# Performance work log

Hardware: AMD Instinct MI355X
Metric: run time of the kernel (lower is better)

The kernel has to match this reference:

```python
import jax, jax.numpy as jnp
import numpy as np

B, T, D, H = 4096, 512, 8, 64  # batch, seq_len, input_size, hidden_size


def setup_inputs() -> dict:
    key = jax.random.key(0)
    ks = jax.random.split(key, 11)
    s = lambda k, shape: (jax.random.normal(k, shape, dtype=jnp.float32) * 0.1)
    return {
        "x": jax.random.normal(ks[0], (B, T, D), dtype=jnp.float32),
        # layer 0 (input_size -> H), PyTorch gate order i,f,g,o packed along 4H
        "Wih0": s(ks[1], (4 * H, D)),
        "Whh0": s(ks[2], (4 * H, H)),
        "bih0": s(ks[3], (4 * H,)),
        "bhh0": s(ks[4], (4 * H,)),
        # layer 1 (H -> H)
        "Wih1": s(ks[5], (4 * H, H)),
        "Whh1": s(ks[6], (4 * H, H)),
        "bih1": s(ks[7], (4 * H,)),
        "bhh1": s(ks[8], (4 * H,)),
        # final linear head H -> 1
        "Wfc": s(ks[9], (1, H)),
        "bfc": s(ks[10], (1,)),
    }


def _lstm_layer(x, Wih, Whh, bih, bhh):
    """Single-direction LSTM layer over x:[B,T,Din] -> hs:[B,T,H]."""
    b, t, _ = x.shape
    h_dim = Whh.shape[1]
    # Precompute input contribution for all timesteps (one big GEMM).
    xg = jnp.einsum("btd,gd->btg", x, Wih) + bih + bhh  # [B,T,4H]

    def step(carry, gx_t):
        h, c = carry
        z = gx_t + h @ Whh.T  # [B,4H]
        i, f, g, o = jnp.split(z, 4, axis=-1)
        i = jax.nn.sigmoid(i)
        f = jax.nn.sigmoid(f)
        g = jnp.tanh(g)
        o = jax.nn.sigmoid(o)
        c = f * c + i * g
        h = o * jnp.tanh(c)
        return (h, c), h

    h0 = jnp.zeros((b, h_dim), x.dtype)
    c0 = jnp.zeros((b, h_dim), x.dtype)
    (_, _), hs = jax.lax.scan(step, (h0, c0), jnp.swapaxes(xg, 0, 1))
    return jnp.swapaxes(hs, 0, 1)  # [B,T,H]


def reference(x, Wih0, Whh0, bih0, bhh0, Wih1, Whh1, bih1, bhh1, Wfc, bfc):
    # nn.LSTM with num_layers=2, batch_first=True; dropout inactive in eval.
    h1 = _lstm_layer(x, Wih0, Whh0, bih0, bhh0)
    h2 = _lstm_layer(h1, Wih1, Whh1, bih1, bhh1)
    last = h2[:, -1, :]  # [B,H]
    return last @ Wfc.T + bfc  # [B,1]
```

## Files before the change

### kernel.cpp

```cpp
#include <hip/hip_runtime.h>

#define BTOT 4096
#define TB   512
#define BD   8
#define BSL  16

#define A0TOG  1024
#define A1BASE 2048
#define A1TOG  1024
#define ZBASE  4096
#define XBASE  8192
#define NLDS   24576

typedef __attribute__((ext_vector_type(8))) short  short8;
typedef __attribute__((ext_vector_type(4))) float  f32x4;

static __device__ __forceinline__ unsigned short f2bf(float f) {
    unsigned u = __float_as_uint(f);
    u += 0x7fffu + ((u >> 16) & 1u);
    return (unsigned short)(u >> 16);
}
static __device__ __forceinline__ float bf2f(unsigned short h) {
    return __uint_as_float(((unsigned)h) << 16);
}
static __device__ __forceinline__ unsigned pkbf(float a, float b) {
    unsigned r;
    asm("v_cvt_pk_bf16_f32 %0, %1, %2" : "=v"(r) : "v"(a), "v"(b));
    return r;
}

static __device__ __forceinline__ void gates4(
    const f32x4 ai, const f32x4 af, const f32x4 ag, const f32x4 ao,
    float cc[4], unsigned hp[2])
{
    float h[4];
    #pragma unroll
    for (int r = 0; r < 4; ++r) {
        const float ei = __builtin_amdgcn_exp2f(ai[r]);
        const float ef = __builtin_amdgcn_exp2f(af[r]);
        const float eg = __builtin_amdgcn_exp2f(ag[r]);
        const float eo = __builtin_amdgcn_exp2f(ao[r]);
        const float Ai = 1.f + ei, Af = 1.f + ef, Ag = 1.f + eg, Ao = 1.f + eo;
        const float P    = Ai * Ag;
        const float numer = cc[r] * P + Af * (eg - 1.f);
        const float rD   = __builtin_amdgcn_rcpf(Af * P);
        cc[r] = numer * rD;
        const float ec = __builtin_amdgcn_exp2f(2.88539008f * cc[r]);
        const float rH = __builtin_amdgcn_rcpf(Ao * (ec + 1.f));
        h[r] = (ec - 1.f) * rH;
    }
    hp[0] = pkbf(h[0], h[1]); hp[1] = pkbf(h[2], h[3]);
}

__global__ __launch_bounds__(512, 2) void lstm2_fused(
    const float* __restrict__ x,
    const float* __restrict__ Wih0, const float* __restrict__ Whh0,
    const float* __restrict__ bih0, const float* __restrict__ bhh0,
    const float* __restrict__ Wih1, const float* __restrict__ Whh1,
    const float* __restrict__ bih1, const float* __restrict__ bhh1,
    const float* __restrict__ Wfc,  const float* __restrict__ bfc,
    float* __restrict__ out)
{
    __shared__ __align__(16) unsigned short lds16[NLDS];

    const int tid  = threadIdx.x;
    const int wid  = tid >> 6;
    const int lane = tid & 63;
    const int q    = lane >> 4;
    const int ln   = lane & 15;
    const int rb   = blockIdx.x * BSL;

    const bool L1w = (wid >= 4);
    const int  g   = L1w ? (wid - 4) : wid;
    const int  jc  = g * 16 + ln;

    const float SCI = -1.44269504f;
    const float SCG =  2.88539008f;
    short8 Bf[4][4];
    #pragma unroll
    for (int G = 0; G < 4; ++G) {
        const int n = G * 64 + jc;
        const float sc = (G == 2) ? SCG : SCI;
        #pragma unroll
        for (int ki = 0; ki < 4; ++ki) {
            union { unsigned short u[8]; short8 v; } t;
            #pragma unroll
            for (int j = 0; j < 8; ++j) {
                const int k = ki * 32 + q * 8 + j;
                float wv = 0.0f;
                if (!L1w) {
                    if (ki < 3) {
                        if (k < 64)      wv = Whh0[n * 64 + k];
                        else if (k < 72) wv = Wih0[n * 8 + (k - 64)];
                    }
                } else {
                    if (k < 64)          wv = Wih1[n * 64 + k];
                    else                 wv = Whh1[n * 64 + (k - 64)];
                }
                t.u[j] = f2bf(sc * wv);
            }
            Bf[G][ki] = t.v;
        }
    }
    f32x4 biasv[4];
    #pragma unroll
    for (int G = 0; G < 4; ++G) {
        const int n = G * 64 + jc;
        const float sc = (G == 2) ? SCG : SCI;
        const float b = sc * (L1w ? (bih1[n] + bhh1[n]) : (bih0[n] + bhh0[n]));
        biasv[G] = (f32x4){b, b, b, b};
    }

    {
        unsigned* z = (unsigned*)lds16;
        #pragma unroll
        for (int i = 0; i < 5; ++i) {
            const int id = tid + i * 512;
            if (id < 2112) z[id] = 0;
        }
    }
    const int srow = tid >> 5, su = tid & 31;
    {
        const float* gp = x + (size_t)(rb + srow) * (TB * BD) + su * 16;
        const float4 v0 = ((const float4*)gp)[0];
        const float4 v1 = ((const float4*)gp)[1];
        const float4 v2 = ((const float4*)gp)[2];
        const float4 v3 = ((const float4*)gp)[3];
        uint4 s0, s1;
        s0.x = pkbf(v0.x, v0.y); s0.y = pkbf(v0.z, v0.w);
        s0.z = pkbf(v1.x, v1.y); s0.w = pkbf(v1.z, v1.w);
        s1.x = pkbf(v2.x, v2.y); s1.y = pkbf(v2.z, v2.w);
        s1.z = pkbf(v3.x, v3.y); s1.w = pkbf(v3.z, v3.w);
        const int el = XBASE + (su * 2) * 128 + srow * 8;
        *(uint4*)(lds16 + el)       = s0;
        *(uint4*)(lds16 + el + 128) = s1;
    }
    __syncthreads();

    const int rbase = q * 128 + ln * 8;
    const int wb    = (jc >> 3) * 128 + q * 32 + (jc & 7);
    const int ln8   = ln * 8;
    const int zaddr = ZBASE + ln8;
    int rdA  = rbase;
    int wr0  = A0TOG + wb;
    int rdH0 = rbase;
    int rdH1 = A1BASE + rbase;
    int wrH1 = A1BASE + A1TOG + wb;

    float cc[4] = {0.f, 0.f, 0.f, 0.f};
    float4 px0, px1, px2, px3;

    for (int it = 0; it <= TB; ++it) {
        const int ph = it & 63;
        if (ph == 48 && it + 16 < TB) {
            const int t0 = (it & ~63) + 64;
            const float* gp = x + (size_t)(rb + srow) * (TB * BD) + t0 * BD + su * 16;
            px0 = ((const float4*)gp)[0];
            px1 = ((const float4*)gp)[1];
            px2 = ((const float4*)gp)[2];
            px3 = ((const float4*)gp)[3];
        }
        if (ph == 62 && it + 2 < TB) {
            const int t0 = (it & ~63) + 64;
            uint4 s0, s1;
            s0.x = pkbf(px0.x, px0.y); s0.y = pkbf(px0.z, px0.w);
            s0.z = pkbf(px1.x, px1.y); s0.w = pkbf(px1.z, px1.w);
            s1.x = pkbf(px2.x, px2.y); s1.y = pkbf(px2.z, px2.w);
            s1.z = pkbf(px3.x, px3.y); s1.w = pkbf(px3.z, px3.w);
            const int el = XBASE + ((t0 & 127) + su * 2) * 128 + srow * 8;
            *(uint4*)(lds16 + el)       = s0;
            *(uint4*)(lds16 + el + 128) = s1;
        }

        if (!L1w) {
            if (it < TB) {
                const short8 a0 = *(const short8*)(lds16 + rdA);
                const short8 a1 = *(const short8*)(lds16 + rdA + 512);
                const int xaddr = (q == 0) ? (XBASE + ((it & 127) << 7) + ln8) : zaddr;
                const short8 a2 = *(const short8*)(lds16 + xaddr);

                f32x4 ai = __builtin_amdgcn_mfma_f32_16x16x32_bf16(a0, Bf[0][0], biasv[0], 0, 0, 0);
                f32x4 af = __builtin_amdgcn_mfma_f32_16x16x32_bf16(a0, Bf[1][0], biasv[1], 0, 0, 0);
                f32x4 ag = __builtin_amdgcn_mfma_f32_16x16x32_bf16(a0, Bf[2][0], biasv[2], 0, 0, 0);
                f32x4 ao = __builtin_amdgcn_mfma_f32_16x16x32_bf16(a0, Bf[3][0], biasv[3], 0, 0, 0);
                ai = __builtin_amdgcn_mfma_f32_16x16x32_bf16(a1, Bf[0][1], ai, 0, 0, 0);
                af = __builtin_amdgcn_mfma_f32_16x16x32_bf16(a1, Bf[1][1], af, 0, 0, 0);
                ag = __builtin_amdgcn_mfma_f32_16x16x32_bf16(a1, Bf[2][1], ag, 0, 0, 0);
                ao = __builtin_amdgcn_mfma_f32_16x16x32_bf16(a1, Bf[3][1], ao, 0, 0, 0);
                ai = __builtin_amdgcn_mfma_f32_16x16x32_bf16(a2, Bf[0][2], ai, 0, 0, 0);
                af = __builtin_amdgcn_mfma_f32_16x16x32_bf16(a2, Bf[1][2], af, 0, 0, 0);
                ag = __builtin_amdgcn_mfma_f32_16x16x32_bf16(a2, Bf[2][2], ag, 0, 0, 0);
                ao = __builtin_amdgcn_mfma_f32_16x16x32_bf16(a2, Bf[3][2], ao, 0, 0, 0);

                unsigned hp[2];
                gates4(ai, af, ag, ao, cc, hp);
                lds16[wr0]      = (unsigned short)hp[0];
                lds16[wr0 + 8]  = (unsigned short)(hp[0] >> 16);
                lds16[wr0 + 16] = (unsigned short)hp[1];
                lds16[wr0 + 24] = (unsigned short)(hp[1] >> 16);
            }
        } else {
            if (it >= 1) {
                const short8 a0 = *(const short8*)(lds16 + rdH0);
                const short8 a1 = *(const short8*)(lds16 + rdH0 + 512);
                const short8 a2 = *(const short8*)(lds16 + rdH1);
                const short8 a3 = *(const short8*)(lds16 + rdH1 + 512);

                f32x4 ai = __builtin_amdgcn_mfma_f32_16x16x32_bf16(a0, Bf[0][0], biasv[0], 0, 0, 0);
                f32x4 af = __builtin_amdgcn_mfma_f32_16x16x32_bf16(a0, Bf[1][0], biasv[1], 0, 0, 0);
                f32x4 ag = __builtin_amdgcn_mfma_f32_16x16x32_bf16(a0, Bf[2][0], biasv[2], 0, 0, 0);
                f32x4 ao = __builtin_amdgcn_mfma_f32_16x16x32_bf16(a0, Bf[3][0], biasv[3], 0, 0, 0);
                ai = __builtin_amdgcn_mfma_f32_16x16x32_bf16(a1, Bf[0][1], ai, 0, 0, 0);
                af = __builtin_amdgcn_mfma_f32_16x16x32_bf16(a1, Bf[1][1], af, 0, 0, 0);
                ag = __builtin_amdgcn_mfma_f32_16x16x32_bf16(a1, Bf[2][1], ag, 0, 0, 0);
                ao = __builtin_amdgcn_mfma_f32_16x16x32_bf16(a1, Bf[3][1], ao, 0, 0, 0);
                ai = __builtin_amdgcn_mfma_f32_16x16x32_bf16(a2, Bf[0][2], ai, 0, 0, 0);
                af = __builtin_amdgcn_mfma_f32_16x16x32_bf16(a2, Bf[1][2], af, 0, 0, 0);
                ag = __builtin_amdgcn_mfma_f32_16x16x32_bf16(a2, Bf[2][2], ag, 0, 0, 0);
                ao = __builtin_amdgcn_mfma_f32_16x16x32_bf16(a2, Bf[3][2], ao, 0, 0, 0);
                ai = __builtin_amdgcn_mfma_f32_16x16x32_bf16(a3, Bf[0][3], ai, 0, 0, 0);
                af = __builtin_amdgcn_mfma_f32_16x16x32_bf16(a3, Bf[1][3], af, 0, 0, 0);
                ag = __builtin_amdgcn_mfma_f32_16x16x32_bf16(a3, Bf[2][3], ag, 0, 0, 0);
                ao = __builtin_amdgcn_mfma_f32_16x16x32_bf16(a3, Bf[3][3], ao, 0, 0, 0);

                unsigned hp[2];
                gates4(ai, af, ag, ao, cc, hp);
                lds16[wrH1]      = (unsigned short)hp[0];
                lds16[wrH1 + 8]  = (unsigned short)(hp[0] >> 16);
                lds16[wrH1 + 16] = (unsigned short)hp[1];
                lds16[wrH1 + 24] = (unsigned short)(hp[1] >> 16);
            }
        }
        __syncthreads();
        rdA ^= A0TOG; wr0 ^= A0TOG; rdH0 ^= A0TOG;
        rdH1 ^= A1TOG; wrH1 ^= A1TOG;
    }

    if (tid < BSL) {
        float s = bfc[0];
        #pragma unroll 8
        for (int j = 0; j < 64; ++j)
            s += bf2f(lds16[A1BASE + A1TOG + (j >> 3) * 128 + tid * 8 + (j & 7)]) * Wfc[j];
        out[rb + tid] = s;
    }
}

extern "C" void kernel_launch(void* const* d_in, const int* in_sizes, int n_in,
                              void* d_out, int out_size, void* d_ws, size_t ws_size,
                              hipStream_t stream) {
    const float* x    = (const float*)d_in[0];
    const float* Wih0 = (const float*)d_in[1];
    const float* Whh0 = (const float*)d_in[2];
    const float* bih0 = (const float*)d_in[3];
    const float* bhh0 = (const float*)d_in[4];
    const float* Wih1 = (const float*)d_in[5];
    const float* Whh1 = (const float*)d_in[6];
    const float* bih1 = (const float*)d_in[7];
    const float* bhh1 = (const float*)d_in[8];
    const float* Wfc  = (const float*)d_in[9];
    const float* bfc  = (const float*)d_in[10];
    float* out = (float*)d_out;

    dim3 grid(BTOT / BSL);
    dim3 block(512);
    lstm2_fused<<<grid, block, 0, stream>>>(x, Wih0, Whh0, bih0, bhh0,
                                            Wih1, Whh1, bih1, bhh1, Wfc, bfc, out);
}
```

Measured before the change: 504.6 us.

## Merge both LSTM layers into each wave with 256-thread blocks and peeled loop

Each wave now computes both layer-0 and layer-1 gates for its hidden-column slice instead of splitting layers across wave groups, which halves the block to 256 threads. The first and last timesteps are peeled out of the loop to remove per-iteration branching. __syncthreads is replaced with an explicit lgkmcnt wait plus s_barrier. The change cuts barrier participants and lets the two layers' MFMA chains interleave within one wave, but it doubles the weight registers per thread and uses launch bounds of one block, so occupancy and register pressure may suffer.

```diff
diff --git a/kernel.cpp b/kernel.cpp
--- a/kernel.cpp
+++ b/kernel.cpp
@@ -14,6 +14,10 @@
 
 typedef __attribute__((ext_vector_type(8))) short  short8;
 typedef __attribute__((ext_vector_type(4))) float  f32x4;
+
+#define MFMA16 __builtin_amdgcn_mfma_f32_16x16x32_bf16
+
+#define BAR() asm volatile("s_waitcnt lgkmcnt(0)\n\ts_barrier" ::: "memory")
 
 static __device__ __forceinline__ unsigned short f2bf(float f) {
     unsigned u = __float_as_uint(f);
@@ -52,7 +56,7 @@
     hp[0] = pkbf(h[0], h[1]); hp[1] = pkbf(h[2], h[3]);
 }
 
-__global__ __launch_bounds__(512, 2) void lstm2_fused(
+__global__ __launch_bounds__(256, 1) void lstm2_fused(
     const float* __restrict__ x,
     const float* __restrict__ Wih0, const float* __restrict__ Whh0,
     const float* __restrict__ bih0, const float* __restrict__ bhh0,
@@ -69,71 +73,76 @@
     const int q    = lane >> 4;
     const int ln   = lane & 15;
     const int rb   = blockIdx.x * BSL;
-
-    const bool L1w = (wid >= 4);
-    const int  g   = L1w ? (wid - 4) : wid;
-    const int  jc  = g * 16 + ln;
+    const int jc   = wid * 16 + ln;
 
     const float SCI = -1.44269504f;
     const float SCG =  2.88539008f;
-    short8 Bf[4][4];
+
+    short8 Bf0[4][3];
+    short8 Bf1[4][4];
     #pragma unroll
     for (int G = 0; G < 4; ++G) {
         const int n = G * 64 + jc;
         const float sc = (G == 2) ? SCG : SCI;
+        #pragma unroll
+        for (int ki = 0; ki < 3; ++ki) {
+            union { unsigned short u[8]; short8 v; } t;
+            #pragma unroll
+            for (int j = 0; j < 8; ++j) {
+                const int k = ki * 32 + q * 8 + j;
+                float wv = 0.0f;
+                if (k < 64)      wv = Whh0[n * 64 + k];
+                else if (k < 72) wv = Wih0[n * 8 + (k - 64)];
+                t.u[j] = f2bf(sc * wv);
+            }
+            Bf0[G][ki] = t.v;
+        }
         #pragma unroll
         for (int ki = 0; ki < 4; ++ki) {
             union { unsigned short u[8]; short8 v; } t;
             #pragma unroll
             for (int j = 0; j < 8; ++j) {
                 const int k = ki * 32 + q * 8 + j;
-                float wv = 0.0f;
-                if (!L1w) {
-                    if (ki < 3) {
-                        if (k < 64)      wv = Whh0[n * 64 + k];
-                        else if (k < 72) wv = Wih0[n * 8 + (k - 64)];
-                    }
-                } else {
-                    if (k < 64)          wv = Wih1[n * 64 + k];
-                    else                 wv = Whh1[n * 64 + (k - 64)];
-                }
+                const float wv = (k < 64) ? Wih1[n * 64 + k]
+                                          : Whh1[n * 64 + (k - 64)];
                 t.u[j] = f2bf(sc * wv);
             }
-            Bf[G][ki] = t.v;
-        }
-    }
-    f32x4 biasv[4];
+            Bf1[G][ki] = t.v;
+        }
+    }
+    f32x4 bias0[4], bias1[4];
     #pragma unroll
     for (int G = 0; G < 4; ++G) {
         const int n = G * 64 + jc;
         const float sc = (G == 2) ? SCG : SCI;
-        const float b = sc * (L1w ? (bih1[n] + bhh1[n]) : (bih0[n] + bhh0[n]));
-        biasv[G] = (f32x4){b, b, b, b};
+        const float b0 = sc * (bih0[n] + bhh0[n]);
+        const float b1 = sc * (bih1[n] + bhh1[n]);
+        bias0[G] = (f32x4){b0, b0, b0, b0};
+        bias1[G] = (f32x4){b1, b1, b1, b1};
     }
 
     {
         unsigned* z = (unsigned*)lds16;
         #pragma unroll
-        for (int i = 0; i < 5; ++i) {
-            const int id = tid + i * 512;
+        for (int i = 0; i < 9; ++i) {
+            const int id = tid + i * 256;
             if (id < 2112) z[id] = 0;
         }
     }
-    const int srow = tid >> 5, su = tid & 31;
+    const int srow = tid >> 4, su = tid & 15;
     {
-        const float* gp = x + (size_t)(rb + srow) * (TB * BD) + su * 16;
-        const float4 v0 = ((const float4*)gp)[0];
-        const float4 v1 = ((const float4*)gp)[1];
-        const float4 v2 = ((const float4*)gp)[2];
-        const float4 v3 = ((const float4*)gp)[3];
-        uint4 s0, s1;
-        s0.x = pkbf(v0.x, v0.y); s0.y = pkbf(v0.z, v0.w);
-        s0.z = pkbf(v1.x, v1.y); s0.w = pkbf(v1.z, v1.w);
-        s1.x = pkbf(v2.x, v2.y); s1.y = pkbf(v2.z, v2.w);
-        s1.z = pkbf(v3.x, v3.y); s1.w = pkbf(v3.z, v3.w);
-        const int el = XBASE + (su * 2) * 128 + srow * 8;
-        *(uint4*)(lds16 + el)       = s0;
-        *(uint4*)(lds16 + el + 128) = s1;
+        const float* gp = x + (size_t)(rb + srow) * (TB * BD) + su * 32;
+        float4 v[8];
+        #pragma unroll
+        for (int i = 0; i < 8; ++i) v[i] = ((const float4*)gp)[i];
+        #pragma unroll
+        for (int tt = 0; tt < 4; ++tt) {
+            uint4 s;
+            s.x = pkbf(v[2*tt].x,   v[2*tt].y);   s.y = pkbf(v[2*tt].z,   v[2*tt].w);
+            s.z = pkbf(v[2*tt+1].x, v[2*tt+1].y); s.w = pkbf(v[2*tt+1].z, v[2*tt+1].w);
+            const int el = XBASE + (su * 4 + tt) * 128 + srow * 8;
+            *(uint4*)(lds16 + el) = s;
+        }
     }
     __syncthreads();
 
@@ -143,97 +152,142 @@
     const int zaddr = ZBASE + ln8;
     int rdA  = rbase;
     int wr0  = A0TOG + wb;
-    int rdH0 = rbase;
     int rdH1 = A1BASE + rbase;
     int wrH1 = A1BASE + A1TOG + wb;
 
-    float cc[4] = {0.f, 0.f, 0.f, 0.f};
-    float4 px0, px1, px2, px3;
-
-    for (int it = 0; it <= TB; ++it) {
+    float cc0[4] = {0.f, 0.f, 0.f, 0.f};
+    float cc1[4] = {0.f, 0.f, 0.f, 0.f};
+    float4 px[8];
+
+    {
+        const short8 a0 = *(const short8*)(lds16 + rdA);
+        const short8 a1 = *(const short8*)(lds16 + rdA + 512);
+        const int xaddr = (q == 0) ? (XBASE + 0 + ln8) : zaddr;
+        const short8 a2 = *(const short8*)(lds16 + xaddr);
+        f32x4 ai = MFMA16(a0, Bf0[0][0], bias0[0], 0, 0, 0);
+        f32x4 af = MFMA16(a0, Bf0[1][0], bias0[1], 0, 0, 0);
+        f32x4 ag = MFMA16(a0, Bf0[2][0], bias0[2], 0, 0, 0);
+        f32x4 ao = MFMA16(a0, Bf0[3][0], bias0[3], 0, 0, 0);
+        ai = MFMA16(a1, Bf0[0][1], ai, 0, 0, 0);
+        af = MFMA16(a1, Bf0[1][1], af, 0, 0, 0);
+        ag = MFMA16(a1, Bf0[2][1], ag, 0, 0, 0);
+        ao = MFMA16(a1, Bf0[3][1], ao, 0, 0, 0);
+        ai = MFMA16(a2, Bf0[0][2], ai, 0, 0, 0);
+        af = MFMA16(a2, Bf0[1][2], af, 0, 0, 0);
+        ag = MFMA16(a2, Bf0[2][2], ag, 0, 0, 0);
+        ao = MFMA16(a2, Bf0[3][2], ao, 0, 0, 0);
+        unsigned hp[2];
+        gates4(ai, af, ag, ao, cc0, hp);
+        lds16[wr0]      = (unsigned short)hp[0];
+        lds16[wr0 + 8]  = (unsigned short)(hp[0] >> 16);
+        lds16[wr0 + 16] = (unsigned short)hp[1];
+        lds16[wr0 + 24] = (unsigned short)(hp[1] >> 16);
+        BAR();
+        rdA ^= A0TOG; wr0 ^= A0TOG; rdH1 ^= A1TOG; wrH1 ^= A1TOG;
+    }
+
+    for (int it = 1; it < TB; ++it) {
         const int ph = it & 63;
         if (ph == 48 && it + 16 < TB) {
             const int t0 = (it & ~63) + 64;
-            const float* gp = x + (size_t)(rb + srow) * (TB * BD) + t0 * BD + su * 16;
-            px0 = ((const float4*)gp)[0];
-            px1 = ((const float4*)gp)[1];
-            px2 = ((const float4*)gp)[2];
-            px3 = ((const float4*)gp)[3];
+            const float* gp = x + (size_t)(rb + srow) * (TB * BD) + t0 * BD + su * 32;
+            #pragma unroll
+            for (int i = 0; i < 8; ++i) px[i] = ((const float4*)gp)[i];
         }
         if (ph == 62 && it + 2 < TB) {
             const int t0 = (it & ~63) + 64;
-            uint4 s0, s1;
-            s0.x = pkbf(px0.x, px0.y); s0.y = pkbf(px0.z, px0.w);
-            s0.z = pkbf(px1.x, px1.y); s0.w = pkbf(px1.z, px1.w);
-            s1.x = pkbf(px2.x, px2.y); s1.y = pkbf(px2.z, px2.w);
-            s1.z = pkbf(px3.x, px3.y); s1.w = pkbf(px3.z, px3.w);
-            const int el = XBASE + ((t0 & 127) + su * 2) * 128 + srow * 8;
-            *(uint4*)(lds16 + el)       = s0;
-            *(uint4*)(lds16 + el + 128) = s1;
-        }
-
-        if (!L1w) {
-            if (it < TB) {
-                const short8 a0 = *(const short8*)(lds16 + rdA);
-                const short8 a1 = *(const short8*)(lds16 + rdA + 512);
-                const int xaddr = (q == 0) ? (XBASE + ((it & 127) << 7) + ln8) : zaddr;
-                const short8 a2 = *(const short8*)(lds16 + xaddr);
-
-                f32x4 ai = __builtin_amdgcn_mfma_f32_16x16x32_bf16(a0, Bf[0][0], biasv[0], 0, 0, 0);
-                f32x4 af = __builtin_amdgcn_mfma_f32_16x16x32_bf16(a0, Bf[1][0], biasv[1], 0, 0, 0);
-                f32x4 ag = __builtin_amdgcn_mfma_f32_16x16x32_bf16(a0, Bf[2][0], biasv[2], 0, 0, 0);
-                f32x4 ao = __builtin_amdgcn_mfma_f32_16x16x32_bf16(a0, Bf[3][0], biasv[3], 0, 0, 0);
-                ai = __builtin_amdgcn_mfma_f32_16x16x32_bf16(a1, Bf[0][1], ai, 0, 0, 0);
-                af = __builtin_amdgcn_mfma_f32_16x16x32_bf16(a1, Bf[1][1], af, 0, 0, 0);
-                ag = __builtin_amdgcn_mfma_f32_16x16x32_bf16(a1, Bf[2][1], ag, 0, 0, 0);
-                ao = __builtin_amdgcn_mfma_f32_16x16x32_bf16(a1, Bf[3][1], ao, 0, 0, 0);
-                ai = __builtin_amdgcn_mfma_f32_16x16x32_bf16(a2, Bf[0][2], ai, 0, 0, 0);
-                af = __builtin_amdgcn_mfma_f32_16x16x32_bf16(a2, Bf[1][2], af, 0, 0, 0);
-                ag = __builtin_amdgcn_mfma_f32_16x16x32_bf16(a2, Bf[2][2], ag, 0, 0, 0);
-                ao = __builtin_amdgcn_mfma_f32_16x16x32_bf16(a2, Bf[3][2], ao, 0, 0, 0);
-
-                unsigned hp[2];
-                gates4(ai, af, ag, ao, cc, hp);
-                lds16[wr0]      = (unsigned short)hp[0];
-                lds16[wr0 + 8]  = (unsigned short)(hp[0] >> 16);
-                lds16[wr0 + 16] = (unsigned short)hp[1];
-                lds16[wr0 + 24] = (unsigned short)(hp[1] >> 16);
+            #pragma unroll
+            for (int tt = 0; tt < 4; ++tt) {
+                uint4 s;
+                s.x = pkbf(px[2*tt].x,   px[2*tt].y);   s.y = pkbf(px[2*tt].z,   px[2*tt].w);
+                s.z = pkbf(px[2*tt+1].x, px[2*tt+1].y); s.w = pkbf(px[2*tt+1].z, px[2*tt+1].w);
+                const int el = XBASE + ((t0 + su * 4 + tt) & 127) * 128 + srow * 8;
+                *(uint4*)(lds16 + el) = s;
             }
-        } else {
-            if (it >= 1) {
-                const short8 a0 = *(const short8*)(lds16 + rdH0);
-                const short8 a1 = *(const short8*)(lds16 + rdH0 + 512);
-                const short8 a2 = *(const short8*)(lds16 + rdH1);
-                const short8 a3 = *(const short8*)(lds16 + rdH1 + 512);
-
-                f32x4 ai = __builtin_amdgcn_mfma_f32_16x16x32_bf16(a0, Bf[0][0], biasv[0], 0, 0, 0);
-                f32x4 af = __builtin_amdgcn_mfma_f32_16x16x32_bf16(a0, Bf[1][0], biasv[1], 0, 0, 0);
-                f32x4 ag = __builtin_amdgcn_mfma_f32_16x16x32_bf16(a0, Bf[2][0], biasv[2], 0, 0, 0);
-                f32x4 ao = __builtin_amdgcn_mfma_f32_16x16x32_bf16(a0, Bf[3][0], biasv[3], 0, 0, 0);
-                ai = __builtin_amdgcn_mfma_f32_16x16x32_bf16(a1, Bf[0][1], ai, 0, 0, 0);
-                af = __builtin_amdgcn_mfma_f32_16x16x32_bf16(a1, Bf[1][1], af, 0, 0, 0);
-                ag = __builtin_amdgcn_mfma_f32_16x16x32_bf16(a1, Bf[2][1], ag, 0, 0, 0);
-                ao = __builtin_amdgcn_mfma_f32_16x16x32_bf16(a1, Bf[3][1], ao, 0, 0, 0);
-                ai = __builtin_amdgcn_mfma_f32_16x16x32_bf16(a2, Bf[0][2], ai, 0, 0, 0);
-                af = __builtin_amdgcn_mfma_f32_16x16x32_bf16(a2, Bf[1][2], af, 0, 0, 0);
-                ag = __builtin_amdgcn_mfma_f32_16x16x32_bf16(a2, Bf[2][2], ag, 0, 0, 0);
-                ao = __builtin_amdgcn_mfma_f32_16x16x32_bf16(a2, Bf[3][2], ao, 0, 0, 0);
-                ai = __builtin_amdgcn_mfma_f32_16x16x32_bf16(a3, Bf[0][3], ai, 0, 0, 0);
-                af = __builtin_amdgcn_mfma_f32_16x16x32_bf16(a3, Bf[1][3], af, 0, 0, 0);
-                ag = __builtin_amdgcn_mfma_f32_16x16x32_bf16(a3, Bf[2][3], ag, 0, 0, 0);
-                ao = __builtin_amdgcn_mfma_f32_16x16x32_bf16(a3, Bf[3][3], ao, 0, 0, 0);
-
-                unsigned hp[2];
-                gates4(ai, af, ag, ao, cc, hp);
-                lds16[wrH1]      = (unsigned short)hp[0];
-                lds16[wrH1 + 8]  = (unsigned short)(hp[0] >> 16);
-                lds16[wrH1 + 16] = (unsigned short)hp[1];
-                lds16[wrH1 + 24] = (unsigned short)(hp[1] >> 16);
-            }
-        }
-        __syncthreads();
-        rdA ^= A0TOG; wr0 ^= A0TOG; rdH0 ^= A0TOG;
-        rdH1 ^= A1TOG; wrH1 ^= A1TOG;
+        }
+
+        const short8 a0 = *(const short8*)(lds16 + rdA);
+        const short8 a1 = *(const short8*)(lds16 + rdA + 512);
+        const short8 b2 = *(const short8*)(lds16 + rdH1);
+        const short8 b3 = *(const short8*)(lds16 + rdH1 + 512);
+        const int xaddr = (q == 0) ? (XBASE + ((it & 127) << 7) + ln8) : zaddr;
+        const short8 a2 = *(const short8*)(lds16 + xaddr);
+
+        f32x4 ai0 = MFMA16(a0, Bf0[0][0], bias0[0], 0, 0, 0);
+        f32x4 af0 = MFMA16(a0, Bf0[1][0], bias0[1], 0, 0, 0);
+        f32x4 ag0 = MFMA16(a0, Bf0[2][0], bias0[2], 0, 0, 0);
+        f32x4 ao0 = MFMA16(a0, Bf0[3][0], bias0[3], 0, 0, 0);
+        ai0 = MFMA16(a1, Bf0[0][1], ai0, 0, 0, 0);
+        af0 = MFMA16(a1, Bf0[1][1], af0, 0, 0, 0);
+        ag0 = MFMA16(a1, Bf0[2][1], ag0, 0, 0, 0);
+        ao0 = MFMA16(a1, Bf0[3][1], ao0, 0, 0, 0);
+        ai0 = MFMA16(a2, Bf0[0][2], ai0, 0, 0, 0);
+        af0 = MFMA16(a2, Bf0[1][2], af0, 0, 0, 0);
+        ag0 = MFMA16(a2, Bf0[2][2], ag0, 0, 0, 0);
+        ao0 = MFMA16(a2, Bf0[3][2], ao0, 0, 0, 0);
+
+        f32x4 ai1 = MFMA16(a0, Bf1[0][0], bias1[0], 0, 0, 0);
+        f32x4 af1 = MFMA16(a0, Bf1[1][0], bias1[1], 0, 0, 0);
+        f32x4 ag1 = MFMA16(a0, Bf1[2][0], bias1[2], 0, 0, 0);
+        f32x4 ao1 = MFMA16(a0, Bf1[3][0], bias1[3], 0, 0, 0);
+        ai1 = MFMA16(a1, Bf1[0][1], ai1, 0, 0, 0);
+        af1 = MFMA16(a1, Bf1[1][1], af1, 0, 0, 0);
+        ag1 = MFMA16(a1, Bf1[2][1], ag1, 0, 0, 0);
+        ao1 = MFMA16(a1, Bf1[3][1], ao1, 0, 0, 0);
+        ai1 = MFMA16(b2, Bf1[0][2], ai1, 0, 0, 0);
+        af1 = MFMA16(b2, Bf1[1][2], af1, 0, 0, 0);
+        ag1 = MFMA16(b2, Bf1[2][2], ag1, 0, 0, 0);
+        ao1 = MFMA16(b2, Bf1[3][2], ao1, 0, 0, 0);
+        ai1 = MFMA16(b3, Bf1[0][3], ai1, 0, 0, 0);
+        af1 = MFMA16(b3, Bf1[1][3], af1, 0, 0, 0);
+        ag1 = MFMA16(b3, Bf1[2][3], ag1, 0, 0, 0);
+        ao1 = MFMA16(b3, Bf1[3][3], ao1, 0, 0, 0);
+
+        unsigned hp0[2], hp1[2];
+        gates4(ai0, af0, ag0, ao0, cc0, hp0);
+        lds16[wr0]      = (unsigned short)hp0[0];
+        lds16[wr0 + 8]  = (unsigned short)(hp0[0] >> 16);
+        lds16[wr0 + 16] = (unsigned short)hp0[1];
+        lds16[wr0 + 24] = (unsigned short)(hp0[1] >> 16);
+
+        gates4(ai1, af1, ag1, ao1, cc1, hp1);
+        lds16[wrH1]      = (unsigned short)hp1[0];
+        lds16[wrH1 + 8]  = (unsigned short)(hp1[0] >> 16);
+        lds16[wrH1 + 16] = (unsigned short)hp1[1];
+        lds16[wrH1 + 24] = (unsigned short)(hp1[1] >> 16);
+
+        BAR();
+        rdA ^= A0TOG; wr0 ^= A0TOG; rdH1 ^= A1TOG; wrH1 ^= A1TOG;
+    }
+
+    {
+        const short8 a0 = *(const short8*)(lds16 + rdA);
+        const short8 a1 = *(const short8*)(lds16 + rdA + 512);
+        const short8 b2 = *(const short8*)(lds16 + rdH1);
+        const short8 b3 = *(const short8*)(lds16 + rdH1 + 512);
+        f32x4 ai = MFMA16(a0, Bf1[0][0], bias1[0], 0, 0, 0);
+        f32x4 af = MFMA16(a0, Bf1[1][0], bias1[1], 0, 0, 0);
+        f32x4 ag = MFMA16(a0, Bf1[2][0], bias1[2], 0, 0, 0);
+        f32x4 ao = MFMA16(a0, Bf1[3][0], bias1[3], 0, 0, 0);
+        ai = MFMA16(a1, Bf1[0][1], ai, 0, 0, 0);
+        af = MFMA16(a1, Bf1[1][1], af, 0, 0, 0);
+        ag = MFMA16(a1, Bf1[2][1], ag, 0, 0, 0);
+        ao = MFMA16(a1, Bf1[3][1], ao, 0, 0, 0);
+        ai = MFMA16(b2, Bf1[0][2], ai, 0, 0, 0);
+        af = MFMA16(b2, Bf1[1][2], af, 0, 0, 0);
+        ag = MFMA16(b2, Bf1[2][2], ag, 0, 0, 0);
+        ao = MFMA16(b2, Bf1[3][2], ao, 0, 0, 0);
+        ai = MFMA16(b3, Bf1[0][3], ai, 0, 0, 0);
+        af = MFMA16(b3, Bf1[1][3], af, 0, 0, 0);
+        ag = MFMA16(b3, Bf1[2][3], ag, 0, 0, 0);
+        ao = MFMA16(b3, Bf1[3][3], ao, 0, 0, 0);
+        unsigned hp[2];
+        gates4(ai, af, ag, ao, cc1, hp);
+        lds16[wrH1]      = (unsigned short)hp[0];
+        lds16[wrH1 + 8]  = (unsigned short)(hp[0] >> 16);
+        lds16[wrH1 + 16] = (unsigned short)hp[1];
+        lds16[wrH1 + 24] = (unsigned short)(hp[1] >> 16);
+        BAR();
     }
 
     if (tid < BSL) {
@@ -262,7 +316,7 @@
     float* out = (float*)d_out;
 
     dim3 grid(BTOT / BSL);
-    dim3 block(512);
+    dim3 block(256);
     lstm2_fused<<<grid, block, 0, stream>>>(x, Wih0, Whh0, bih0, bhh0,
                                             Wih1, Whh1, bih1, bhh1, Wfc, bfc, out);
 }
```

New measurement: 503.6 us. No clear change (-0.2%).

## Split LSTM step into MFMA and gate phases, interleaving layer-0 and layer-1 waves

Applied to the files above, without the earlier changes.

Each time step now has two barrier-separated phases. Layer-0 waves run their MFMAs in the first phase and gate math in the second, while layer-1 waves do the reverse, so matrix and transcendental work from the two layers overlap across waves. The layer-1 pipeline is skewed by one more step, and __syncthreads is replaced with an explicit lgkmcnt wait plus s_barrier. In exchange there are two barriers per step instead of one, the loop runs one extra iteration, and the accumulator registers stay live across the barrier.

```diff
diff --git a/kernel.cpp b/kernel.cpp
--- a/kernel.cpp
+++ b/kernel.cpp
@@ -14,6 +14,10 @@
 
 typedef __attribute__((ext_vector_type(8))) short  short8;
 typedef __attribute__((ext_vector_type(4))) float  f32x4;
+
+#define MFMA16 __builtin_amdgcn_mfma_f32_16x16x32_bf16
+
+#define BAR() asm volatile("s_waitcnt lgkmcnt(0)\n\ts_barrier" ::: "memory")
 
 static __device__ __forceinline__ unsigned short f2bf(float f) {
     unsigned u = __float_as_uint(f);
@@ -76,6 +80,7 @@
 
     const float SCI = -1.44269504f;
     const float SCG =  2.88539008f;
+
     short8 Bf[4][4];
     #pragma unroll
     for (int G = 0; G < 4; ++G) {
@@ -143,25 +148,56 @@
     const int zaddr = ZBASE + ln8;
     int rdA  = rbase;
     int wr0  = A0TOG + wb;
-    int rdH0 = rbase;
     int rdH1 = A1BASE + rbase;
-    int wrH1 = A1BASE + A1TOG + wb;
+    int wrH1 = A1BASE + wb;
 
     float cc[4] = {0.f, 0.f, 0.f, 0.f};
     float4 px0, px1, px2, px3;
-
-    for (int it = 0; it <= TB; ++it) {
-        const int ph = it & 63;
-        if (ph == 48 && it + 16 < TB) {
-            const int t0 = (it & ~63) + 64;
+    f32x4 ai0, af0, ag0, ao0;
+    f32x4 ai1, af1, ag1, ao1;
+
+    for (int t = 0; t < TB + 2; ++t) {
+        const int ph = t & 63;
+        if (ph == 48 && t + 16 < TB) {
+            const int t0 = (t & ~63) + 64;
             const float* gp = x + (size_t)(rb + srow) * (TB * BD) + t0 * BD + su * 16;
             px0 = ((const float4*)gp)[0];
             px1 = ((const float4*)gp)[1];
             px2 = ((const float4*)gp)[2];
             px3 = ((const float4*)gp)[3];
         }
-        if (ph == 62 && it + 2 < TB) {
-            const int t0 = (it & ~63) + 64;
+
+        if (!L1w) {
+            if (t < TB) {
+                const short8 a0 = *(const short8*)(lds16 + rdA);
+                const short8 a1 = *(const short8*)(lds16 + rdA + 512);
+                const int xaddr = (q == 0) ? (XBASE + ((t & 127) << 7) + ln8) : zaddr;
+                const short8 a2 = *(const short8*)(lds16 + xaddr);
+                ai0 = MFMA16(a0, Bf[0][0], biasv[0], 0, 0, 0);
+                af0 = MFMA16(a0, Bf[1][0], biasv[1], 0, 0, 0);
+                ag0 = MFMA16(a0, Bf[2][0], biasv[2], 0, 0, 0);
+                ao0 = MFMA16(a0, Bf[3][0], biasv[3], 0, 0, 0);
+                ai0 = MFMA16(a1, Bf[0][1], ai0, 0, 0, 0);
+                af0 = MFMA16(a1, Bf[1][1], af0, 0, 0, 0);
+                ag0 = MFMA16(a1, Bf[2][1], ag0, 0, 0, 0);
+                ao0 = MFMA16(a1, Bf[3][1], ao0, 0, 0, 0);
+                ai0 = MFMA16(a2, Bf[0][2], ai0, 0, 0, 0);
+                af0 = MFMA16(a2, Bf[1][2], af0, 0, 0, 0);
+                ag0 = MFMA16(a2, Bf[2][2], ag0, 0, 0, 0);
+                ao0 = MFMA16(a2, Bf[3][2], ao0, 0, 0, 0);
+            }
+        } else {
+            if (t >= 2) {
+                unsigned hp[2];
+                gates4(ai1, af1, ag1, ao1, cc, hp);
+                lds16[wrH1]      = (unsigned short)hp[0];
+                lds16[wrH1 + 8]  = (unsigned short)(hp[0] >> 16);
+                lds16[wrH1 + 16] = (unsigned short)hp[1];
+                lds16[wrH1 + 24] = (unsigned short)(hp[1] >> 16);
+            }
+        }
+        if (ph == 62 && t + 2 < TB) {
+            const int t0 = (t & ~63) + 64;
             uint4 s0, s1;
             s0.x = pkbf(px0.x, px0.y); s0.y = pkbf(px0.z, px0.w);
             s0.z = pkbf(px1.x, px1.y); s0.w = pkbf(px1.z, px1.w);
@@ -171,69 +207,43 @@
             *(uint4*)(lds16 + el)       = s0;
             *(uint4*)(lds16 + el + 128) = s1;
         }
+        BAR();
 
         if (!L1w) {
-            if (it < TB) {
-                const short8 a0 = *(const short8*)(lds16 + rdA);
-                const short8 a1 = *(const short8*)(lds16 + rdA + 512);
-                const int xaddr = (q == 0) ? (XBASE + ((it & 127) << 7) + ln8) : zaddr;
-                const short8 a2 = *(const short8*)(lds16 + xaddr);
-
-                f32x4 ai = __builtin_amdgcn_mfma_f32_16x16x32_bf16(a0, Bf[0][0], biasv[0], 0, 0, 0);
-                f32x4 af = __builtin_amdgcn_mfma_f32_16x16x32_bf16(a0, Bf[1][0], biasv[1], 0, 0, 0);
-                f32x4 ag = __builtin_amdgcn_mfma_f32_16x16x32_bf16(a0, Bf[2][0], biasv[2], 0, 0, 0);
-                f32x4 ao = __builtin_amdgcn_mfma_f32_16x16x32_bf16(a0, Bf[3][0], biasv[3], 0, 0, 0);
-                ai = __builtin_amdgcn_mfma_f32_16x16x32_bf16(a1, Bf[0][1], ai, 0, 0, 0);
-                af = __builtin_amdgcn_mfma_f32_16x16x32_bf16(a1, Bf[1][1], af, 0, 0, 0);
-                ag = __builtin_amdgcn_mfma_f32_16x16x32_bf16(a1, Bf[2][1], ag, 0, 0, 0);
-                ao = __builtin_amdgcn_mfma_f32_16x16x32_bf16(a1, Bf[3][1], ao, 0, 0, 0);
-                ai = __builtin_amdgcn_mfma_f32_16x16x32_bf16(a2, Bf[0][2], ai, 0, 0, 0);
-                af = __builtin_amdgcn_mfma_f32_16x16x32_bf16(a2, Bf[1][2], af, 0, 0, 0);
-                ag = __builtin_amdgcn_mfma_f32_16x16x32_bf16(a2, Bf[2][2], ag, 0, 0, 0);
-                ao = __builtin_amdgcn_mfma_f32_16x16x32_bf16(a2, Bf[3][2], ao, 0, 0, 0);
-
+            if (t < TB) {
                 unsigned hp[2];
-                gates4(ai, af, ag, ao, cc, hp);
+                gates4(ai0, af0, ag0, ao0, cc, hp);
                 lds16[wr0]      = (unsigned short)hp[0];
                 lds16[wr0 + 8]  = (unsigned short)(hp[0] >> 16);
                 lds16[wr0 + 16] = (unsigned short)hp[1];
                 lds16[wr0 + 24] = (unsigned short)(hp[1] >> 16);
             }
         } else {
-            if (it >= 1) {
-                const short8 a0 = *(const short8*)(lds16 + rdH0);
-                const short8 a1 = *(const short8*)(lds16 + rdH0 + 512);
-                const short8 a2 = *(const short8*)(lds16 + rdH1);
-                const short8 a3 = *(const short8*)(lds16 + rdH1 + 512);
-
-                f32x4 ai = __builtin_amdgcn_mfma_f32_16x16x32_bf16(a0, Bf[0][0], biasv[0], 0, 0, 0);
-                f32x4 af = __builtin_amdgcn_mfma_f32_16x16x32_bf16(a0, Bf[1][0], biasv[1], 0, 0, 0);
-                f32x4 ag = __builtin_amdgcn_mfma_f32_16x16x32_bf16(a0, Bf[2][0], biasv[2], 0, 0, 0);
-                f32x4 ao = __builtin_amdgcn_mfma_f32_16x16x32_bf16(a0, Bf[3][0], biasv[3], 0, 0, 0);
-                ai = __builtin_amdgcn_mfma_f32_16x16x32_bf16(a1, Bf[0][1], ai, 0, 0, 0);
-                af = __builtin_amdgcn_mfma_f32_16x16x32_bf16(a1, Bf[1][1], af, 0, 0, 0);
-                ag = __builtin_amdgcn_mfma_f32_16x16x32_bf16(a1, Bf[2][1], ag, 0, 0, 0);
-                ao = __builtin_amdgcn_mfma_f32_16x16x32_bf16(a1, Bf[3][1], ao, 0, 0, 0);
-                ai = __builtin_amdgcn_mfma_f32_16x16x32_bf16(a2, Bf[0][2], ai, 0, 0, 0);
-                af = __builtin_amdgcn_mfma_f32_16x16x32_bf16(a2, Bf[1][2], af, 0, 0, 0);
-                ag = __builtin_amdgcn_mfma_f32_16x16x32_bf16(a2, Bf[2][2], ag, 0, 0, 0);
-                ao = __builtin_amdgcn_mfma_f32_16x16x32_bf16(a2, Bf[3][2], ao, 0, 0, 0);
-                ai = __builtin_amdgcn_mfma_f32_16x16x32_bf16(a3, Bf[0][3], ai, 0, 0, 0);
-                af = __builtin_amdgcn_mfma_f32_16x16x32_bf16(a3, Bf[1][3], af, 0, 0, 0);
-                ag = __builtin_amdgcn_mfma_f32_16x16x32_bf16(a3, Bf[2][3], ag, 0, 0, 0);
-                ao = __builtin_amdgcn_mfma_f32_16x16x32_bf16(a3, Bf[3][3], ao, 0, 0, 0);
-
-                unsigned hp[2];
-                gates4(ai, af, ag, ao, cc, hp);
-                lds16[wrH1]      = (unsigned short)hp[0];
-                lds16[wrH1 + 8]  = (unsigned short)(hp[0] >> 16);
-                lds16[wrH1 + 16] = (unsigned short)hp[1];
-                lds16[wrH1 + 24] = (unsigned short)(hp[1] >> 16);
-            }
-        }
-        __syncthreads();
-        rdA ^= A0TOG; wr0 ^= A0TOG; rdH0 ^= A0TOG;
-        rdH1 ^= A1TOG; wrH1 ^= A1TOG;
+            if (t >= 1 && t <= TB) {
+                const short8 a0 = *(const short8*)(lds16 + rdA);
+                const short8 a1 = *(const short8*)(lds16 + rdA + 512);
+                const short8 b2 = *(const short8*)(lds16 + rdH1);
+                const short8 b3 = *(const short8*)(lds16 + rdH1 + 512);
+                ai1 = MFMA16(a0, Bf[0][0], biasv[0], 0, 0, 0);
+                af1 = MFMA16(a0, Bf[1][0], biasv[1], 0, 0, 0);
+                ag1 = MFMA16(a0, Bf[2][0], biasv[2], 0, 0, 0);
+                ao1 = MFMA16(a0, Bf[3][0], biasv[3], 0, 0, 0);
+                ai1 = MFMA16(a1, Bf[0][1], ai1, 0, 0, 0);
+                af1 = MFMA16(a1, Bf[1][1], af1, 0, 0, 0);
+                ag1 = MFMA16(a1, Bf[2][1], ag1, 0, 0, 0);
+                ao1 = MFMA16(a1, Bf[3][1], ao1, 0, 0, 0);
+                ai1 = MFMA16(b2, Bf[0][2], ai1, 0, 0, 0);
+                af1 = MFMA16(b2, Bf[1][2], af1, 0, 0, 0);
+                ag1 = MFMA16(b2, Bf[2][2], ag1, 0, 0, 0);
+                ao1 = MFMA16(b2, Bf[3][2], ao1, 0, 0, 0);
+                ai1 = MFMA16(b3, Bf[0][3], ai1, 0, 0, 0);
+                af1 = MFMA16(b3, Bf[1][3], af1, 0, 0, 0);
+                ag1 = MFMA16(b3, Bf[2][3], ag1, 0, 0, 0);
+                ao1 = MFMA16(b3, Bf[3][3], ao1, 0, 0, 0);
+            }
+        }
+        BAR();
+        rdA ^= A0TOG; wr0 ^= A0TOG; rdH1 ^= A1TOG; wrH1 ^= A1TOG;
     }
 
     if (tid < BSL) {
```

Result: slower. 545.3 us (+8.1%).
